# Kernel optimization log

Hardware: AMD Instinct MI355X
Metric: run time of the kernel (lower is better)

Reference implementation:

```python
import jax, jax.numpy as jnp
import numpy as np

SLOPE = 10.0  # surrogate gradient sigmoid slope

@jax.custom_vjp
def surrogate_spike(u):
    # forward: Heaviside step (u > 0)
    return (u > 0).astype(u.dtype)

def _spike_fwd(u):
    return surrogate_spike(u), u

def _spike_bwd(u, g):
    s = jax.nn.sigmoid(SLOPE * u)
    return (g * SLOPE * s * (1.0 - s),)

surrogate_spike.defvjp(_spike_fwd, _spike_bwd)

V_RESET = 0.0


def setup_inputs() -> dict:
    key = jax.random.key(0)
    T, B, N = 64, 64, 16384
    x_seq = jax.random.normal(key, (T, B, N), dtype=jnp.float32)
    return {
        "x_seq": x_seq,
        "v_th": jnp.asarray(1.0, dtype=jnp.float32),
        "tau": jnp.asarray(2.0, dtype=jnp.float32),
    }


def reference(x_seq, v_th, tau):
    # PmLIF membrane recurrence over T timesteps.
    # h_t = v_{t-1} + (1/tau) * (-(v_{t-1} - v_reset) + x_t)
    # s_t = Heaviside(h_t - v_th)   (surrogate grad in bwd)
    # v_t = h_t * (1 - s_t) + v_reset * s_t
    def step(v, x):
        h = v + (1.0 / tau) * (-(v - V_RESET) + x)
        s = surrogate_spike(h - v_th)
        v_new = h * (1.0 - s) + V_RESET * s
        return v_new, s

    v0 = jnp.zeros_like(x_seq[0])
    _, spikes = jax.lax.scan(step, v0, x_seq)
    return spikes  # [T, B, N]
```

## Files before the change

kernel.cpp:

```cpp
#include <hip/hip_runtime.h>


constexpr int T_STEPS = 64;

typedef float f32x2 __attribute__((ext_vector_type(2)));

struct StepOut { float v; float s; };

__device__ __forceinline__ StepOut pmlif_step(float xv, float v,
                                              float inv_tau, float v_th) {
    const float t = __fsub_rn(xv, v);
    const float h = __fadd_rn(v, __fmul_rn(inv_tau, t));
    const float u = __fsub_rn(h, v_th);
    const bool  b = u > 0.0f;
    StepOut r;
    r.s = b ? 1.0f : 0.0f;
    r.v = b ? 0.0f : h;
    return r;
}

__global__ __launch_bounds__(256, 8) void pmlif_scan_kernel(
    const f32x2* __restrict__ x,
    f32x2* __restrict__ out,
    const float* __restrict__ v_th_p,
    const float* __restrict__ tau_p,
    int n2)
{
    const int idx = blockIdx.x * blockDim.x + threadIdx.x;
    if (idx >= n2) return;

    const float v_th    = *v_th_p;
    const float inv_tau = __fdiv_rn(1.0f, *tau_p);

    const f32x2* __restrict__ xp = x + idx;
    f32x2* __restrict__ op = out + idx;
    const size_t step = (size_t)n2;

    float v0 = 0.f, v1 = 0.f;

#pragma unroll
    for (int t = 0; t < T_STEPS; ++t) {
        const f32x2 xv = __builtin_nontemporal_load(&xp[(size_t)t * step]);
        const StepOut r0 = pmlif_step(xv.x, v0, inv_tau, v_th);
        const StepOut r1 = pmlif_step(xv.y, v1, inv_tau, v_th);
        v0 = r0.v; v1 = r1.v;
        f32x2 s; s.x = r0.s; s.y = r1.s;
        __builtin_nontemporal_store(s, &op[(size_t)t * step]);
    }
}

extern "C" void kernel_launch(void* const* d_in, const int* in_sizes, int n_in,
                              void* d_out, int out_size, void* d_ws, size_t ws_size,
                              hipStream_t stream) {
    const float* x    = (const float*)d_in[0];
    const float* v_th = (const float*)d_in[1];
    const float* tau  = (const float*)d_in[2];
    float* out = (float*)d_out;

    const int total = in_sizes[0];
    const int bn    = total / T_STEPS;
    const int n2    = bn / 2;

    const int block = 256;
    const int grid  = (n2 + block - 1) / block;

    pmlif_scan_kernel<<<grid, block, 0, stream>>>(
        (const f32x2*)x, (f32x2*)out, v_th, tau, n2);
}
```

Before: 118.8 us.

## Use 128-bit loads with lane-pair shuffles and explicit register prefetch pipeline

Each thread pair now splits time steps: even lanes load 16 bytes at even steps and odd lanes at odd steps, then swap halves with shuffles so each thread still owns two neurons across all steps. This widens memory transactions from 64-bit to 128-bit. A software prefetch buffer of four loads ahead is added to raise memory-level parallelism. The cost is extra shuffles and selects per step and more registers under an 8-waves launch bound.

```diff
diff --git a/kernel.cpp b/kernel.cpp
--- a/kernel.cpp
+++ b/kernel.cpp
@@ -2,8 +2,12 @@
 
 
 constexpr int T_STEPS = 64;
+constexpr int NPAIR   = T_STEPS / 2;
+constexpr int PF      = 4;
+constexpr int NGRP    = NPAIR / PF;
 
 typedef float f32x2 __attribute__((ext_vector_type(2)));
+typedef float f32x4 __attribute__((ext_vector_type(4)));
 
 struct StepOut { float v; float s; };
 
@@ -20,32 +24,74 @@
 }
 
 __global__ __launch_bounds__(256, 8) void pmlif_scan_kernel(
-    const f32x2* __restrict__ x,
-    f32x2* __restrict__ out,
+    const float* __restrict__ x,
+    float* __restrict__ out,
     const float* __restrict__ v_th_p,
     const float* __restrict__ tau_p,
-    int n2)
+    int bn)
 {
-    const int idx = blockIdx.x * blockDim.x + threadIdx.x;
-    if (idx >= n2) return;
+    const int idx2 = blockIdx.x * blockDim.x + threadIdx.x;
+    const int n2   = bn >> 1;
+    if (idx2 >= n2) return;
+
+    const int  q4  = idx2 >> 1;
+    const bool odd = (threadIdx.x & 1);
 
     const float v_th    = *v_th_p;
     const float inv_tau = __fdiv_rn(1.0f, *tau_p);
 
-    const f32x2* __restrict__ xp = x + idx;
-    f32x2* __restrict__ op = out + idx;
-    const size_t step = (size_t)n2;
+    const float* __restrict__ xb = x   + (size_t)(odd ? 1 : 0) * bn + (size_t)q4 * 4;
+    float* __restrict__ ob       = out + (size_t)(odd ? 1 : 0) * bn + (size_t)q4 * 4;
+    const size_t ps = (size_t)2 * bn;
+
+    f32x4 buf[PF];
+#pragma unroll
+    for (int k = 0; k < PF; ++k)
+        buf[k] = __builtin_nontemporal_load(
+            reinterpret_cast<const f32x4*>(xb + (size_t)k * ps));
 
     float v0 = 0.f, v1 = 0.f;
 
+    for (int g = 0; g < NGRP; ++g) {
+        const float* __restrict__ xg = xb + (size_t)(g + 1) * PF * ps;
+        float* __restrict__ og       = ob + (size_t)g * PF * ps;
 #pragma unroll
-    for (int t = 0; t < T_STEPS; ++t) {
-        const f32x2 xv = __builtin_nontemporal_load(&xp[(size_t)t * step]);
-        const StepOut r0 = pmlif_step(xv.x, v0, inv_tau, v_th);
-        const StepOut r1 = pmlif_step(xv.y, v1, inv_tau, v_th);
-        v0 = r0.v; v1 = r1.v;
-        f32x2 s; s.x = r0.s; s.y = r1.s;
-        __builtin_nontemporal_store(s, &op[(size_t)t * step]);
+        for (int k = 0; k < PF; ++k) {
+            const f32x4 V = buf[k];
+            if (g + 1 < NGRP)
+                buf[k] = __builtin_nontemporal_load(
+                    reinterpret_cast<const f32x4*>(xg + (size_t)k * ps));
+
+            const float sx = odd ? V.x : V.z;
+            const float sy = odd ? V.y : V.w;
+            const float rx = __shfl_xor(sx, 1, 64);
+            const float ry = __shfl_xor(sy, 1, 64);
+
+            const float x0a = odd ? rx  : V.x;
+            const float x0b = odd ? ry  : V.y;
+            const float x1a = odd ? V.z : rx;
+            const float x1b = odd ? V.w : ry;
+
+            const StepOut a0 = pmlif_step(x0a, v0, inv_tau, v_th);
+            const StepOut b0 = pmlif_step(x0b, v1, inv_tau, v_th);
+            const StepOut a1 = pmlif_step(x1a, a0.v, inv_tau, v_th);
+            const StepOut b1 = pmlif_step(x1b, b0.v, inv_tau, v_th);
+            v0 = a1.v; v1 = b1.v;
+
+            const float tx = odd ? a0.s : a1.s;
+            const float ty = odd ? b0.s : b1.s;
+            const float ux = __shfl_xor(tx, 1, 64);
+            const float uy = __shfl_xor(ty, 1, 64);
+
+            f32x4 st;
+            st.x = odd ? ux   : a0.s;
+            st.y = odd ? uy   : b0.s;
+            st.z = odd ? a1.s : ux;
+            st.w = odd ? b1.s : uy;
+
+            __builtin_nontemporal_store(
+                st, reinterpret_cast<f32x4*>(og + (size_t)k * ps));
+        }
     }
 }
 
@@ -64,6 +110,5 @@
     const int block = 256;
     const int grid  = (n2 + block - 1) / block;
 
-    pmlif_scan_kernel<<<grid, block, 0, stream>>>(
-        (const f32x2*)x, (f32x2*)out, v_th, tau, n2);
+    pmlif_scan_kernel<<<grid, block, 0, stream>>>(x, out, v_th, tau, bn);
 }
```

Result: faster. 104.1 us (-12.3%).

## Split kernel into producer/consumer warps with double-buffered LDS staging

Applied to the files above, without the earlier changes.

Replaces the per-thread streaming scan with a warp-specialized design: half the block loads input rows (4 timesteps per phase, float4) into a double-buffered shared-memory ring while the other half runs the recurrence and stores spikes. The intent is to overlap global loads with compute and stores, and to widen accesses to 16 bytes. In exchange it halves the number of threads issuing global loads, adds a block-wide barrier every phase, and adds an LDS round trip. Grid size assumes bn is divisible by 512.

```diff
diff --git a/kernel.cpp b/kernel.cpp
--- a/kernel.cpp
+++ b/kernel.cpp
@@ -1,9 +1,13 @@
 #include <hip/hip_runtime.h>
 
 
-constexpr int T_STEPS = 64;
+constexpr int T_STEPS   = 64;
+constexpr int ROWS_PH   = 4;
+constexpr int NPHASE    = T_STEPS / ROWS_PH;
+constexpr int COLS_BLK  = 512;
+constexpr int CONS_THR  = 128;
 
-typedef float f32x2 __attribute__((ext_vector_type(2)));
+typedef float f32x4 __attribute__((ext_vector_type(4)));
 
 struct StepOut { float v; float s; };
 
@@ -19,33 +23,74 @@
     return r;
 }
 
-__global__ __launch_bounds__(256, 8) void pmlif_scan_kernel(
-    const f32x2* __restrict__ x,
-    f32x2* __restrict__ out,
+__global__ __launch_bounds__(256, 8) void pmlif_pc_kernel(
+    const float* __restrict__ x,
+    float* __restrict__ out,
     const float* __restrict__ v_th_p,
     const float* __restrict__ tau_p,
-    int n2)
+    int bn)
 {
-    const int idx = blockIdx.x * blockDim.x + threadIdx.x;
-    if (idx >= n2) return;
+    __shared__ f32x4 lds[2][ROWS_PH][CONS_THR];
+
+    const int    tid      = threadIdx.x;
+    const bool   producer = tid < 128;
+    const size_t colbase  = (size_t)blockIdx.x * COLS_BLK;
 
     const float v_th    = *v_th_p;
     const float inv_tau = __fdiv_rn(1.0f, *tau_p);
 
-    const f32x2* __restrict__ xp = x + idx;
-    f32x2* __restrict__ op = out + idx;
-    const size_t step = (size_t)n2;
+    if (producer) {
+        const int i = tid;
+        const float* __restrict__ gp = x + colbase + (size_t)i * 4;
 
-    float v0 = 0.f, v1 = 0.f;
+        {
+            f32x4 a = __builtin_nontemporal_load((const f32x4*)(gp + (size_t)0 * bn));
+            f32x4 b = __builtin_nontemporal_load((const f32x4*)(gp + (size_t)1 * bn));
+            f32x4 c = __builtin_nontemporal_load((const f32x4*)(gp + (size_t)2 * bn));
+            f32x4 d = __builtin_nontemporal_load((const f32x4*)(gp + (size_t)3 * bn));
+            lds[0][0][i] = a; lds[0][1][i] = b; lds[0][2][i] = c; lds[0][3][i] = d;
+        }
+        __syncthreads();
 
+        for (int p = 0; p < NPHASE; ++p) {
+            if (p + 1 < NPHASE) {
+                const float* __restrict__ gb = gp + (size_t)(p + 1) * ROWS_PH * bn;
+                f32x4 a = __builtin_nontemporal_load((const f32x4*)(gb + (size_t)0 * bn));
+                f32x4 b = __builtin_nontemporal_load((const f32x4*)(gb + (size_t)1 * bn));
+                f32x4 c = __builtin_nontemporal_load((const f32x4*)(gb + (size_t)2 * bn));
+                f32x4 d = __builtin_nontemporal_load((const f32x4*)(gb + (size_t)3 * bn));
+                const int nb = (p + 1) & 1;
+                lds[nb][0][i] = a; lds[nb][1][i] = b; lds[nb][2][i] = c; lds[nb][3][i] = d;
+            }
+            __syncthreads();
+        }
+    } else {
+        const int j = tid - 128;
+        float* __restrict__ op = out + colbase + (size_t)j * 4;
+
+        float va = 0.f, vb = 0.f, vc = 0.f, vd = 0.f;
+
+        __syncthreads();
+
+        for (int p = 0; p < NPHASE; ++p) {
+            const int cb = p & 1;
 #pragma unroll
-    for (int t = 0; t < T_STEPS; ++t) {
-        const f32x2 xv = __builtin_nontemporal_load(&xp[(size_t)t * step]);
-        const StepOut r0 = pmlif_step(xv.x, v0, inv_tau, v_th);
-        const StepOut r1 = pmlif_step(xv.y, v1, inv_tau, v_th);
-        v0 = r0.v; v1 = r1.v;
-        f32x2 s; s.x = r0.s; s.y = r1.s;
-        __builtin_nontemporal_store(s, &op[(size_t)t * step]);
+            for (int r = 0; r < ROWS_PH; ++r) {
+                const f32x4 xv = lds[cb][r][j];
+
+                const StepOut s0 = pmlif_step(xv.x, va, inv_tau, v_th);
+                const StepOut s1 = pmlif_step(xv.y, vb, inv_tau, v_th);
+                const StepOut s2 = pmlif_step(xv.z, vc, inv_tau, v_th);
+                const StepOut s3 = pmlif_step(xv.w, vd, inv_tau, v_th);
+                va = s0.v; vb = s1.v; vc = s2.v; vd = s3.v;
+
+                f32x4 s;
+                s.x = s0.s; s.y = s1.s; s.z = s2.s; s.w = s3.s;
+                __builtin_nontemporal_store(
+                    s, (f32x4*)(op + (size_t)(p * ROWS_PH + r) * bn));
+            }
+            __syncthreads();
+        }
     }
 }
 
@@ -59,11 +104,9 @@
 
     const int total = in_sizes[0];
     const int bn    = total / T_STEPS;
-    const int n2    = bn / 2;
 
     const int block = 256;
-    const int grid  = (n2 + block - 1) / block;
+    const int grid  = bn / COLS_BLK;
 
-    pmlif_scan_kernel<<<grid, block, 0, stream>>>(
-        (const f32x2*)x, (f32x2*)out, v_th, tau, n2);
+    pmlif_pc_kernel<<<grid, block, 0, stream>>>(x, out, v_th, tau, bn);
 }
```

Measured after the change: 103.0 us. -13.2%, faster.
